# Kernel optimization log

Hardware: AMD Instinct MI355X
Metric: run time of the kernel (lower is better)

## Reference

```python
import jax, jax.numpy as jnp
import numpy as np
import math

B, P, L, LMAX = 8, 64, 32, 2048
IN_DIM, TE_DIM = 12, 20
POINT = IN_DIM + TE_DIM  # 32
HID = 128
TTCN = HID - 1  # 127
NHEAD = 4
NLAYER = 2
DFF = 2048  # torch TransformerEncoderLayer default dim_feedforward
NQ = 5
TAU = 300.0
DELTA = 5.0 * 60.0  # delta_minutes=5 -> seconds


def _pe_table(M, D):
    pos = np.arange(M, dtype=np.float32)[:, None]
    div = np.exp(np.arange(0, D, 2, dtype=np.float32) * (-math.log(10000.0) / D))
    pe = np.zeros((M, D), np.float32)
    pe[:, 0::2] = np.sin(pos * div)
    pe[:, 1::2] = np.cos(pos * div)
    return jnp.asarray(pe)


def _time_bias(M):
    idx = np.arange(M, dtype=np.float32)
    dist = np.abs(idx[:, None] - idx[None, :]) * DELTA
    return jnp.asarray(np.log(np.exp(-dist / TAU) + 1e-12).astype(np.float32))


def _ln(x, g, b):
    m = jnp.mean(x, axis=-1, keepdims=True)
    v = jnp.var(x, axis=-1, keepdims=True)
    return (x - m) * jax.lax.rsqrt(v + 1e-5) * g + b


def _mha(qx, kx, vx, Wq, bq, Wk, bk, Wv, bv, Wo, bo, bias=None, key_pad=None):
    Bq, Mq, D = qx.shape
    Mk = kx.shape[1]
    dh = D // NHEAD
    q = (qx @ Wq + bq).reshape(Bq, Mq, NHEAD, dh).transpose(0, 2, 1, 3)
    k = (kx @ Wk + bk).reshape(Bq, Mk, NHEAD, dh).transpose(0, 2, 1, 3)
    v = (vx @ Wv + bv).reshape(Bq, Mk, NHEAD, dh).transpose(0, 2, 1, 3)
    s = jnp.einsum('bhqd,bhkd->bhqk', q, k) / math.sqrt(dh)
    if bias is not None:
        s = s + bias[None, None]
    if key_pad is not None:
        s = jnp.where(key_pad[:, None, None, :], -1e9, s)
    a = jax.nn.softmax(s, axis=-1)
    o = jnp.einsum('bhqk,bhkd->bhqd', a, v).transpose(0, 2, 1, 3).reshape(Bq, Mq, D)
    return o @ Wo + bo


def forward_fn(data_sequence, ts_sequence, patch_mask, patch_index, num_batch,
               te_scale_W, te_scale_b, te_per_W, te_per_b,
               fg_W1, fg_b1, fg_W2, fg_b2, fg_W3, fg_b3, T_bias,
               ga_Wq, ga_bq, ga_Wk, ga_bk, ga_Wv, ga_bv, ga_Wo, ga_bo,
               tf_Wq, tf_bq, tf_Wk, tf_bk, tf_Wv, tf_bv, tf_Wo, tf_bo,
               tf_ln1_g, tf_ln1_b, tf_ff_W1, tf_ff_b1, tf_ff_W2, tf_ff_b2,
               tf_ln2_g, tf_ln2_b,
               cls_query, cls_Wq, cls_bq, cls_Wk, cls_bk, cls_Wv, cls_bv,
               cls_Wo, cls_bo, cls_out_W, cls_out_b):
    # --- patchify_by_len, vectorized: per-patch lengths -> cumsum starts + gather ---
    mvalid = patch_mask > 0
    lens = jnp.where(mvalid, jnp.maximum(patch_index, 0), 0)
    starts = jnp.cumsum(lens, axis=1) - lens  # exclusive cumsum (B,P)
    lar = jnp.arange(L)
    idx = starts[:, :, None] + lar[None, None, :]  # (B,P,L)
    valid = (lar[None, None, :] < lens[:, :, None]) & (idx < num_batch[:, None, None]) & mvalid[:, :, None]
    idx_c = jnp.clip(idx, 0, LMAX - 1).reshape(B, P * L)
    Xg = jnp.take_along_axis(data_sequence, idx_c[:, :, None], axis=1).reshape(B, P, L, IN_DIM)
    tsg = jnp.take_along_axis(ts_sequence, idx_c, axis=1).reshape(B, P, L, 1)
    mask_pt = valid.astype(jnp.float32)[..., None]  # (B,P,L,1)
    X_patch = Xg * mask_pt
    ts_patch = tsg * mask_pt
    # --- LearnableTE ---
    te = jnp.concatenate([ts_patch @ te_scale_W + te_scale_b,
                          jnp.sin(ts_patch @ te_per_W + te_per_b)], axis=-1)
    X_int = jnp.concatenate([X_patch, te], axis=-1).reshape(B * P, L, POINT)
    mask2 = mask_pt.reshape(B * P, L, 1)
    # --- TTCN: MLP-generated dynamic filters, masked softmax over timesteps ---
    h = jax.nn.relu(X_int @ fg_W1 + fg_b1)
    h = jax.nn.relu(h @ fg_W2 + fg_b2)
    Filt = h @ fg_W3 + fg_b3  # (N, L, TTCN*POINT)
    Fm = Filt * mask2 + (1.0 - mask2) * -1e8
    Fs = jax.nn.softmax(Fm, axis=1).reshape(B * P, L, TTCN, POINT)
    ttcn = jnp.einsum('nlp,nltp->nt', X_int, Fs)
    h_t = jax.nn.relu(ttcn + T_bias)
    patch_exists = (jnp.sum(mask2, axis=1) > 0).astype(jnp.float32)  # (N,1)
    x = jnp.concatenate([h_t, patch_exists], axis=-1).reshape(B, P, HID)
    # --- stacked time-biased patch attention + transformer encoder ---
    tb = _time_bias(P)
    pe = _pe_table(P, HID)
    key_pad = patch_mask <= 0
    pm = patch_mask[:, :, None]
    for l in range(NLAYER):
        x_last = x
        ga = _mha(x, x, x, ga_Wq[l], ga_bq[l], ga_Wk[l], ga_bk[l],
                  ga_Wv[l], ga_bv[l], ga_Wo[l], ga_bo[l], bias=tb, key_pad=key_pad)
        x = x + ga * pm
        x = x + pe[None]
        # post-norm TransformerEncoderLayer, tf_layer=1, dropout=0 at inference
        a = _mha(x, x, x, tf_Wq[l], tf_bq[l], tf_Wk[l], tf_bk[l],
                 tf_Wv[l], tf_bv[l], tf_Wo[l], tf_bo[l])
        x = _ln(x + a, tf_ln1_g[l], tf_ln1_b[l])
        f = jax.nn.relu(x @ tf_ff_W1[l] + tf_ff_b1[l]) @ tf_ff_W2[l] + tf_ff_b2[l]
        x = _ln(x + f, tf_ln2_g[l], tf_ln2_b[l])
        x = x_last + x
        x = x * pm
    # --- 5-query cross-attention classifier ---
    q = jnp.broadcast_to(cls_query[None], (B, NQ, HID))
    z = _mha(q, x, x, cls_Wq, cls_bq, cls_Wk, cls_bk, cls_Wv, cls_bv,
             cls_Wo, cls_bo, key_pad=key_pad)
    logits = (z @ cls_out_W + cls_out_b)[..., 0]  # (B,5)
    return logits


def setup_inputs() -> dict:
    key = jax.random.key(0)
    ks = iter(jax.random.split(key, 64))
    def nrm(shape, s=0.05):
        return (jax.random.normal(next(ks), shape) * s).astype(jnp.float32)
    inp = {}
    inp['data_sequence'] = jax.random.normal(next(ks), (B, LMAX, IN_DIM), dtype=jnp.float32)
    inp['ts_sequence'] = jax.random.uniform(next(ks), (B, LMAX), dtype=jnp.float32) * 100.0
    inp['patch_mask'] = jnp.ones((B, P), jnp.float32)
    inp['patch_index'] = jax.random.randint(next(ks), (B, P), 1, L + 1)
    inp['num_batch'] = jnp.full((B,), LMAX, jnp.int32)
    inp['te_scale_W'] = nrm((1, 1), 0.5)
    inp['te_scale_b'] = nrm((1,), 0.5)
    inp['te_per_W'] = nrm((1, TE_DIM - 1), 0.5)
    inp['te_per_b'] = nrm((TE_DIM - 1,), 0.5)
    inp['fg_W1'] = nrm((POINT, TTCN)); inp['fg_b1'] = jnp.zeros((TTCN,), jnp.float32)
    inp['fg_W2'] = nrm((TTCN, TTCN)); inp['fg_b2'] = jnp.zeros((TTCN,), jnp.float32)
    inp['fg_W3'] = nrm((TTCN, POINT * TTCN)); inp['fg_b3'] = jnp.zeros((POINT * TTCN,), jnp.float32)
    inp['T_bias'] = nrm((1, TTCN), 0.5)
    for nm in ['ga_Wq', 'ga_Wk', 'ga_Wv', 'ga_Wo', 'tf_Wq', 'tf_Wk', 'tf_Wv', 'tf_Wo']:
        inp[nm] = nrm((NLAYER, HID, HID))
    for nm in ['ga_bq', 'ga_bk', 'ga_bv', 'ga_bo', 'tf_bq', 'tf_bk', 'tf_bv', 'tf_bo', 'tf_ff_b2']:
        inp[nm] = jnp.zeros((NLAYER, HID), jnp.float32)
    inp['tf_ln1_g'] = jnp.ones((NLAYER, HID), jnp.float32)
    inp['tf_ln1_b'] = jnp.zeros((NLAYER, HID), jnp.float32)
    inp['tf_ln2_g'] = jnp.ones((NLAYER, HID), jnp.float32)
    inp['tf_ln2_b'] = jnp.zeros((NLAYER, HID), jnp.float32)
    inp['tf_ff_W1'] = nrm((NLAYER, HID, DFF))
    inp['tf_ff_b1'] = jnp.zeros((NLAYER, DFF), jnp.float32)
    inp['tf_ff_W2'] = nrm((NLAYER, DFF, HID))
    inp['cls_query'] = nrm((NQ, HID), 0.5)
    for nm in ['cls_Wq', 'cls_Wk', 'cls_Wv', 'cls_Wo']:
        inp[nm] = nrm((HID, HID))
    for nm in ['cls_bq', 'cls_bk', 'cls_bv', 'cls_bo']:
        inp[nm] = jnp.zeros((HID,), jnp.float32)
    inp['cls_out_W'] = nrm((HID, 1))
    inp['cls_out_b'] = jnp.zeros((1,), jnp.float32)
    return inp


def reference(data_sequence, ts_sequence, patch_mask, patch_index, num_batch,
              te_scale_W, te_scale_b, te_per_W, te_per_b,
              fg_W1, fg_b1, fg_W2, fg_b2, fg_W3, fg_b3, T_bias,
              ga_Wq, ga_bq, ga_Wk, ga_bk, ga_Wv, ga_bv, ga_Wo, ga_bo,
              tf_Wq, tf_bq, tf_Wk, tf_bk, tf_Wv, tf_bv, tf_Wo, tf_bo,
              tf_ln1_g, tf_ln1_b, tf_ff_W1, tf_ff_b1, tf_ff_W2, tf_ff_b2,
              tf_ln2_g, tf_ln2_b,
              cls_query, cls_Wq, cls_bq, cls_Wk, cls_bk, cls_Wv, cls_bv,
              cls_Wo, cls_bo, cls_out_W, cls_out_b):
    return forward_fn(data_sequence, ts_sequence, patch_mask, patch_index, num_batch,
                      te_scale_W, te_scale_b, te_per_W, te_per_b,
                      fg_W1, fg_b1, fg_W2, fg_b2, fg_W3, fg_b3, T_bias,
                      ga_Wq, ga_bq, ga_Wk, ga_bk, ga_Wv, ga_bv, ga_Wo, ga_bo,
                      tf_Wq, tf_bq, tf_Wk, tf_bk, tf_Wv, tf_bv, tf_Wo, tf_bo,
                      tf_ln1_g, tf_ln1_b, tf_ff_W1, tf_ff_b1, tf_ff_W2, tf_ff_b2,
                      tf_ln2_g, tf_ln2_b,
                      cls_query, cls_Wq, cls_bq, cls_Wk, cls_bk, cls_Wv, cls_bv,
                      cls_Wo, cls_bo, cls_out_W, cls_out_b)
```

## Files before the change

kernel.cpp:

```cpp
#include <hip/hip_runtime.h>
#include <math.h>

#define BB 8
#define PP 64
#define LL 32
#define LMAXX 2048
#define INDIM 12
#define PNT 32
#define HIDD 128
#define TTCNN 127
#define NPATCH 512

#define EPI_NONE 0
#define EPI_RELU 1
#define EPI_GA   2
#define EPI_LN   3
#define EPI_LNF  4

typedef __attribute__((ext_vector_type(8))) short short8v;
typedef __attribute__((ext_vector_type(4))) float float4v;

__device__ inline unsigned short f2bf(float f) {
    unsigned int u = __float_as_uint(f);
    unsigned int r = (u + 0x7FFFu + ((u >> 16) & 1u)) >> 16;
    return (unsigned short)r;
}

__global__ void tables_kernel(float* __restrict__ tb, float* __restrict__ pe)
{
    int e = blockIdx.x*256 + threadIdx.x;
    if (e < 64*64) {
        int i = e >> 6, j = e & 63;
        float dist = fabsf((float)(i - j)) * (300.0f / 300.0f);
        tb[e] = logf(expf(-dist) + 1e-12f);
    } else if (e < 64*64 + 64*128) {
        int e2 = e - 64*64;
        int i = e2 >> 7, d = e2 & 127;
        int mm = d >> 1;
        float div = expf((float)(2*mm) * (-logf(10000.f)/128.f));
        float ang = (float)i * div;
        pe[e2] = (d & 1) ? cosf(ang) : sinf(ang);
    }
}

__global__ void w3t_kernel(const float* __restrict__ W3, unsigned short* __restrict__ W3TB)
{
    int e = blockIdx.x*256 + threadIdx.x;
    if (e >= 4096*128) return;
    int kk = e >> 12, cidx = e & 4095;
    float v = (kk < TTCNN && cidx < 4064) ? W3[kk*4064 + cidx] : 0.f;
    W3TB[cidx*128 + kk] = f2bf(v);
}

__global__ void prep_h2_kernel(const float* __restrict__ data, const float* __restrict__ ts,
                               const float* __restrict__ pmask, const int* __restrict__ pindex,
                               const int* __restrict__ nbatch,
                               const float* __restrict__ teW, const float* __restrict__ teB,
                               const float* __restrict__ tePW, const float* __restrict__ tePB,
                               const float* __restrict__ W1, const float* __restrict__ b1,
                               const float* __restrict__ W2, const float* __restrict__ b2,
                               float* __restrict__ xint, float* __restrict__ maskout,
                               unsigned short* __restrict__ h2o)
{
    int n = blockIdx.x;
    int b = n >> 6, p = n & 63;
    __shared__ int s_start, s_len;
    __shared__ float s_mk[LL];
    __shared__ alignas(16) float Xs[LL*36];
    __shared__ alignas(16) float H1[LL*128];
    int tid = threadIdx.x;
    if (tid == 0) {
        int start = 0;
        for (int j = 0; j < p; ++j) {
            float mv = pmask[b*PP + j];
            int pi = pindex[b*PP + j];
            start += (mv > 0.f) ? (pi > 0 ? pi : 0) : 0;
        }
        float mvp = pmask[b*PP + p];
        int pip = pindex[b*PP + p];
        s_len = (mvp > 0.f) ? (pip > 0 ? pip : 0) : 0;
        s_start = start;
    }
    __syncthreads();
    int start = s_start, len = s_len, nb2 = nbatch[b];
    if (tid < LL) {
        int l = tid;
        int idx = start + l;
        float v = (l < len && idx < nb2) ? 1.f : 0.f;
        s_mk[l] = v;
        maskout[n*LL + l] = v;
    }
    __syncthreads();
    for (int e = tid; e < LL*PNT; e += 128) {
        int l = e >> 5, d = e & 31;
        float mv = s_mk[l];
        int idx = start + l;
        if (idx < 0) idx = 0;
        if (idx > LMAXX-1) idx = LMAXX-1;
        float val;
        if (d < INDIM) {
            val = (mv > 0.f) ? data[(b*LMAXX + idx)*INDIM + d] : 0.f;
        } else {
            float tsm = (mv > 0.f) ? ts[b*LMAXX + idx] : 0.f;
            if (d == INDIM) val = tsm * teW[0] + teB[0];
            else { int j = d - INDIM - 1; val = sinf(tsm * tePW[j] + tePB[j]); }
        }
        Xs[l*36 + d] = val;
        xint[n*(LL*PNT) + e] = val;
    }
    __syncthreads();
    int j = tid;
    float acc[LL];
    if (j < TTCNN) {
        #pragma unroll
        for (int l = 0; l < LL; ++l) acc[l] = b1[j];
        for (int d4 = 0; d4 < 8; ++d4) {
            float w0 = W1[(d4*4+0)*TTCNN + j];
            float w1 = W1[(d4*4+1)*TTCNN + j];
            float w2 = W1[(d4*4+2)*TTCNN + j];
            float w3 = W1[(d4*4+3)*TTCNN + j];
            #pragma unroll
            for (int l = 0; l < LL; ++l) {
                float4 x = *(float4*)&Xs[l*36 + d4*4];
                acc[l] = fmaf(x.x, w0, acc[l]);
                acc[l] = fmaf(x.y, w1, acc[l]);
                acc[l] = fmaf(x.z, w2, acc[l]);
                acc[l] = fmaf(x.w, w3, acc[l]);
            }
        }
        #pragma unroll
        for (int l = 0; l < LL; ++l) H1[l*128 + j] = fmaxf(acc[l], 0.f);
    } else {
        #pragma unroll
        for (int l = 0; l < LL; ++l) H1[l*128 + 127] = 0.f;
    }
    __syncthreads();
    if (j < TTCNN) {
        #pragma unroll
        for (int l = 0; l < LL; ++l) acc[l] = b2[j];
        for (int k4 = 0; k4 < 32; ++k4) {
            int k = k4*4;
            float w0 = W2[(k+0)*TTCNN + j];
            float w1 = W2[(k+1)*TTCNN + j];
            float w2 = W2[(k+2)*TTCNN + j];
            float w3 = (k+3 < TTCNN) ? W2[(k+3)*TTCNN + j] : 0.f;
            #pragma unroll
            for (int l = 0; l < LL; ++l) {
                float4 h = *(float4*)&H1[l*128 + k];
                acc[l] = fmaf(h.x, w0, acc[l]);
                acc[l] = fmaf(h.y, w1, acc[l]);
                acc[l] = fmaf(h.z, w2, acc[l]);
                acc[l] = fmaf(h.w, w3, acc[l]);
            }
        }
        #pragma unroll
        for (int l = 0; l < LL; ++l) h2o[(n*LL + l)*128 + j] = f2bf(fmaxf(acc[l], 0.f));
    } else {
        #pragma unroll
        for (int l = 0; l < LL; ++l) h2o[(n*LL + l)*128 + 127] = 0;
    }
}

__global__ __launch_bounds__(256) void ttcn_mfma_kernel(
    const unsigned short* __restrict__ h2b,
    const float* __restrict__ xint,
    const float* __restrict__ mask,
    const unsigned short* __restrict__ w3tb,
    const float* __restrict__ b3,
    const float* __restrict__ tbias,
    float* __restrict__ x)
{
    int bid = blockIdx.x;
    int n = bid >> 3, chunk = bid & 7;
    __shared__ alignas(16) unsigned short h2s[32*136];
    __shared__ alignas(16) float Xs[32*36];
    __shared__ float mk[32];
    int tid = threadIdx.x;
    for (int f = tid; f < 512; f += 256) {
        int l = f >> 4, c16 = f & 15;
        *(short8v*)&h2s[l*136 + c16*8] = *(const short8v*)&h2b[(n*32 + l)*128 + c16*8];
    }
    {
        int l = tid >> 3, d4 = (tid & 7)*4;
        *(float4*)&Xs[l*36 + d4] = *(const float4*)&xint[n*1024 + l*32 + d4];
    }
    if (tid < 32) mk[tid] = mask[n*32 + tid];
    __syncthreads();
    if (chunk == 0 && tid == 0) {
        float e = 0.f;
        for (int l = 0; l < 32; ++l) e += mk[l];
        x[n*HIDD + 127] = (e > 0.f) ? 1.f : 0.f;
    }
    int wave = tid >> 6, lane = tid & 63;
    int li = lane & 15, hi = lane >> 4;
    short8v a[2][4];
    #pragma unroll
    for (int mt = 0; mt < 2; ++mt)
        #pragma unroll
        for (int kk = 0; kk < 4; ++kk)
            a[mt][kk] = *(short8v*)&h2s[(mt*16 + li)*136 + kk*32 + hi*8];
    int cwbase = chunk*512 + wave*128;
    for (int tl = 0; tl < 4; ++tl) {
        int c0 = cwbase + tl*32;
        float4v acc[2][2] = {};
        #pragma unroll
        for (int nt2 = 0; nt2 < 2; ++nt2) {
            const unsigned short* bp = &w3tb[(size_t)(c0 + nt2*16 + li)*128 + hi*8];
            #pragma unroll
            for (int kk = 0; kk < 4; ++kk) {
                short8v bf = *(const short8v*)&bp[kk*32];
                acc[0][nt2] = __builtin_amdgcn_mfma_f32_16x16x32_bf16(a[0][kk], bf, acc[0][nt2], 0, 0, 0);
                acc[1][nt2] = __builtin_amdgcn_mfma_f32_16x16x32_bf16(a[1][kk], bf, acc[1][nt2], 0, 0, 0);
            }
        }
        int t = c0 >> 5;
        float colv2 = 0.f;
        #pragma unroll
        for (int nt2 = 0; nt2 < 2; ++nt2) {
            int c = c0 + nt2*16 + li;
            float bv = (c < 4064) ? b3[c] : 0.f;
            int p = (nt2 << 4) + li;
            float fm[8];
            #pragma unroll
            for (int mt = 0; mt < 2; ++mt)
                #pragma unroll
                for (int r4 = 0; r4 < 4; ++r4) {
                    int r = mt*16 + hi*4 + r4;
                    float mv = mk[r];
                    fm[mt*4 + r4] = (acc[mt][nt2][r4] + bv)*mv + (1.f - mv)*(-1e8f);
                }
            float m = fm[0];
            #pragma unroll
            for (int i = 1; i < 8; ++i) m = fmaxf(m, fm[i]);
            m = fmaxf(m, __shfl_xor(m, 16));
            m = fmaxf(m, __shfl_xor(m, 32));
            float s = 0.f, w = 0.f;
            #pragma unroll
            for (int mt = 0; mt < 2; ++mt)
                #pragma unroll
                for (int r4 = 0; r4 < 4; ++r4) {
                    int r = mt*16 + hi*4 + r4;
                    float e = expf(fm[mt*4 + r4] - m);
                    s += e;
                    w += e * Xs[r*36 + p];
                }
            s += __shfl_xor(s, 16); w += __shfl_xor(w, 16);
            s += __shfl_xor(s, 32); w += __shfl_xor(w, 32);
            colv2 += w / s;
        }
        colv2 += __shfl_xor(colv2, 1);
        colv2 += __shfl_xor(colv2, 2);
        colv2 += __shfl_xor(colv2, 4);
        colv2 += __shfl_xor(colv2, 8);
        if (lane == 0 && t < TTCNN)
            x[n*HIDD + t] = fmaxf(colv2 + tbias[t], 0.f);
    }
}

__global__ __launch_bounds__(256) void lin_kernel(
    const float* __restrict__ A, int lda,
    const float* __restrict__ W0, const float* __restrict__ Wb0,
    const float* __restrict__ W1, const float* __restrict__ Wb1,
    const float* __restrict__ W2, const float* __restrict__ Wb2,
    float* __restrict__ O0, float* __restrict__ O1, float* __restrict__ O2,
    int M, int K, int N, int epi,
    const float* __restrict__ xres, const float* __restrict__ xlast_in,
    float* __restrict__ xlast_out,
    const float* __restrict__ pmk, const float* __restrict__ pe,
    const float* __restrict__ g, const float* __restrict__ bt)
{
    __shared__ alignas(16) float As[8*68];
    __shared__ float red[4][4][2];
    int tid = threadIdx.x;
    int cloc = tid & 127, rh = tid >> 7;
    int c = blockIdx.z*128 + cloc;
    int r0 = blockIdx.x*8;
    const float* W; const float* Wb; float* O;
    if (blockIdx.y == 0)      { W = W0; Wb = Wb0; O = O0; }
    else if (blockIdx.y == 1) { W = W1; Wb = Wb1; O = O1; }
    else                      { W = W2; Wb = Wb2; O = O2; }
    float acc0 = 0.f, acc1 = 0.f, acc2 = 0.f, acc3 = 0.f;
    for (int kc = 0; kc < K; kc += 64) {
        __syncthreads();
        if (tid < 128) {
            int row = tid >> 4, kk = (tid & 15)*4;
            int r = r0 + row;
            float4 v = make_float4(0.f, 0.f, 0.f, 0.f);
            if (r < M) v = *(const float4*)&A[(size_t)r*lda + kc + kk];
            *(float4*)&As[row*68 + kk] = v;
        }
        __syncthreads();
        const float* wp = &W[(size_t)kc*N + c];
        #pragma unroll 4
        for (int kk4 = 0; kk4 < 16; ++kk4) {
            float w0 = wp[(size_t)(kk4*4+0)*N];
            float w1 = wp[(size_t)(kk4*4+1)*N];
            float w2 = wp[(size_t)(kk4*4+2)*N];
            float w3 = wp[(size_t)(kk4*4+3)*N];
            float4 a0 = *(float4*)&As[(rh*4+0)*68 + kk4*4];
            float4 a1 = *(float4*)&As[(rh*4+1)*68 + kk4*4];
            float4 a2 = *(float4*)&As[(rh*4+2)*68 + kk4*4];
            float4 a3 = *(float4*)&As[(rh*4+3)*68 + kk4*4];
            acc0 += a0.x*w0 + a0.y*w1 + a0.z*w2 + a0.w*w3;
            acc1 += a1.x*w0 + a1.y*w1 + a1.z*w2 + a1.w*w3;
            acc2 += a2.x*w0 + a2.y*w1 + a2.z*w2 + a2.w*w3;
            acc3 += a3.x*w0 + a3.y*w1 + a3.z*w2 + a3.w*w3;
        }
    }
    float bv = Wb ? Wb[c] : 0.f;
    float val[4] = {acc0 + bv, acc1 + bv, acc2 + bv, acc3 + bv};
    int rbase = r0 + rh*4;
    if (epi == EPI_NONE || epi == EPI_RELU) {
        #pragma unroll
        for (int i = 0; i < 4; ++i) {
            int r = rbase + i;
            if (r < M) {
                float v = val[i];
                if (epi == EPI_RELU) v = fmaxf(v, 0.f);
                O[(size_t)r*N + c] = v;
            }
        }
    } else if (epi == EPI_GA) {
        #pragma unroll
        for (int i = 0; i < 4; ++i) {
            int r = rbase + i;
            float xr = xres[r*128 + cloc];
            float pmv = pmk[r];
            float pev = pe[(r & 63)*128 + cloc];
            xlast_out[r*128 + cloc] = xr;
            O[r*128 + cloc] = xr + val[i]*pmv + pev;
        }
    } else {
        float tv[4], s[4], s2[4];
        #pragma unroll
        for (int i = 0; i < 4; ++i) {
            int r = rbase + i;
            tv[i] = xres[r*128 + cloc] + val[i];
            s[i] = tv[i];
            s2[i] = tv[i]*tv[i];
        }
        #pragma unroll
        for (int i = 0; i < 4; ++i) {
            for (int off = 32; off >= 1; off >>= 1) {
                s[i]  += __shfl_xor(s[i],  off);
                s2[i] += __shfl_xor(s2[i], off);
            }
        }
        int wid = tid >> 6;
        if ((tid & 63) == 0) {
            #pragma unroll
            for (int i = 0; i < 4; ++i) { red[wid][i][0] = s[i]; red[wid][i][1] = s2[i]; }
        }
        __syncthreads();
        int pw = wid ^ 1;
        #pragma unroll
        for (int i = 0; i < 4; ++i) {
            float st  = red[wid][i][0] + red[pw][i][0];
            float s2t = red[wid][i][1] + red[pw][i][1];
            float mean = st * (1.f/128.f);
            float var = s2t * (1.f/128.f) - mean*mean;
            float rs = rsqrtf(var + 1e-5f);
            float y = (tv[i] - mean)*rs*g[cloc] + bt[cloc];
            int r = rbase + i;
            if (epi == EPI_LN) O[r*128 + cloc] = y;
            else               O[r*128 + cloc] = (xlast_in[r*128 + cloc] + y)*pmk[r];
        }
    }
}

__global__ __launch_bounds__(256) void ff2_partial_kernel(
    const float* __restrict__ A,
    const float* __restrict__ W,
    float* __restrict__ PART)
{
    __shared__ alignas(16) float As[8*68];
    int tid = threadIdx.x;
    int cloc = tid & 127, rh = tid >> 7;
    int r0 = blockIdx.x*8;
    int kz = blockIdx.z*256;
    float acc0 = 0.f, acc1 = 0.f, acc2 = 0.f, acc3 = 0.f;
    for (int kc = kz; kc < kz + 256; kc += 64) {
        __syncthreads();
        if (tid < 128) {
            int row = tid >> 4, kk = (tid & 15)*4;
            *(float4*)&As[row*68 + kk] = *(const float4*)&A[(size_t)(r0+row)*2048 + kc + kk];
        }
        __syncthreads();
        const float* wp = &W[(size_t)kc*128 + cloc];
        #pragma unroll 4
        for (int kk4 = 0; kk4 < 16; ++kk4) {
            float w0 = wp[(size_t)(kk4*4+0)*128];
            float w1 = wp[(size_t)(kk4*4+1)*128];
            float w2 = wp[(size_t)(kk4*4+2)*128];
            float w3 = wp[(size_t)(kk4*4+3)*128];
            float4 a0 = *(float4*)&As[(rh*4+0)*68 + kk4*4];
            float4 a1 = *(float4*)&As[(rh*4+1)*68 + kk4*4];
            float4 a2 = *(float4*)&As[(rh*4+2)*68 + kk4*4];
            float4 a3 = *(float4*)&As[(rh*4+3)*68 + kk4*4];
            acc0 += a0.x*w0 + a0.y*w1 + a0.z*w2 + a0.w*w3;
            acc1 += a1.x*w0 + a1.y*w1 + a1.z*w2 + a1.w*w3;
            acc2 += a2.x*w0 + a2.y*w1 + a2.z*w2 + a2.w*w3;
            acc3 += a3.x*w0 + a3.y*w1 + a3.z*w2 + a3.w*w3;
        }
    }
    float* pb = &PART[((size_t)blockIdx.z*512 + r0 + rh*4)*128 + cloc];
    pb[0]     = acc0;
    pb[128]   = acc1;
    pb[256]   = acc2;
    pb[384]   = acc3;
}

__global__ void ln2f_kernel(const float* __restrict__ PART, const float* __restrict__ b2,
                            const float* __restrict__ xres, const float* __restrict__ xlast,
                            const float* __restrict__ pmk,
                            const float* __restrict__ g, const float* __restrict__ bt,
                            float* __restrict__ xout)
{
    int r = blockIdx.x, c = threadIdx.x;
    float v = b2[c];
    #pragma unroll
    for (int z = 0; z < 8; ++z) v += PART[((size_t)z*512 + r)*128 + c];
    float tv = xres[r*128 + c] + v;
    float s = tv, s2 = tv*tv;
    for (int off = 32; off >= 1; off >>= 1) {
        s  += __shfl_xor(s,  off);
        s2 += __shfl_xor(s2, off);
    }
    __shared__ float red[2][2];
    int w = c >> 6;
    if ((c & 63) == 0) { red[w][0] = s; red[w][1] = s2; }
    __syncthreads();
    float st  = red[0][0] + red[1][0];
    float s2t = red[0][1] + red[1][1];
    float mean = st * (1.f/128.f);
    float var = s2t * (1.f/128.f) - mean*mean;
    float y = (tv - mean)*rsqrtf(var + 1e-5f)*g[c] + bt[c];
    xout[r*128 + c] = (xlast[r*128 + c] + y)*pmk[r];
}

__global__ __launch_bounds__(256) void attn_kernel(
    const float* __restrict__ q, const float* __restrict__ k, const float* __restrict__ v,
    float* __restrict__ out, const float* __restrict__ tb,
    const float* __restrict__ pmk, int flags)
{
    int bid = blockIdx.x;
    int b = bid >> 3, h = (bid >> 1) & 3, half = bid & 1;
    int rbase = half*32;
    __shared__ alignas(16) float qs[32*36];
    __shared__ alignas(16) float ks[64*36];
    __shared__ alignas(16) float vs[64*36];
    __shared__ float as_[32*68];
    int tid = threadIdx.x;
    {
        int m = tid >> 3, d4 = (tid & 7)*4;
        *(float4*)&qs[m*36 + d4] = *(const float4*)&q[(b*64 + rbase + m)*128 + h*32 + d4];
    }
    for (int f = tid; f < 512; f += 256) {
        int m = f >> 3, d4 = (f & 7)*4;
        int gofs = (b*64 + m)*128 + h*32 + d4;
        *(float4*)&ks[m*36 + d4] = *(const float4*)&k[gofs];
        *(float4*)&vs[m*36 + d4] = *(const float4*)&v[gofs];
    }
    __syncthreads();
    int r = tid >> 3, qd = tid & 7;
    float sreg[8];
    #pragma unroll
    for (int j = 0; j < 8; ++j) {
        int cc = j*8 + qd;
        float acc = 0.f;
        #pragma unroll
        for (int d4 = 0; d4 < 8; ++d4) {
            float4 a = *(float4*)&qs[r*36 + d4*4];
            float4 bb = *(float4*)&ks[cc*36 + d4*4];
            acc += a.x*bb.x + a.y*bb.y + a.z*bb.z + a.w*bb.w;
        }
        float s = acc * 0.17677669529663687f;
        if (flags & 1) s += tb[(rbase + r)*64 + cc];
        if (flags & 2) { if (pmk[b*64 + cc] <= 0.f) s = -1e9f; }
        sreg[j] = s;
    }
    float m = sreg[0];
    #pragma unroll
    for (int j = 1; j < 8; ++j) m = fmaxf(m, sreg[j]);
    m = fmaxf(m, __shfl_xor(m, 1));
    m = fmaxf(m, __shfl_xor(m, 2));
    m = fmaxf(m, __shfl_xor(m, 4));
    float ssum = 0.f;
    #pragma unroll
    for (int j = 0; j < 8; ++j) { sreg[j] = expf(sreg[j] - m); ssum += sreg[j]; }
    ssum += __shfl_xor(ssum, 1);
    ssum += __shfl_xor(ssum, 2);
    ssum += __shfl_xor(ssum, 4);
    float inv = 1.f / ssum;
    #pragma unroll
    for (int j = 0; j < 8; ++j) as_[r*68 + j*8 + qd] = sreg[j]*inv;
    __syncthreads();
    float o0 = 0.f, o1 = 0.f, o2 = 0.f, o3 = 0.f;
    int d0 = qd*4;
    for (int cc = 0; cc < 64; ++cc) {
        float a = as_[r*68 + cc];
        float4 v4 = *(float4*)&vs[cc*36 + d0];
        o0 += a*v4.x; o1 += a*v4.y; o2 += a*v4.z; o3 += a*v4.w;
    }
    *(float4*)&out[(b*64 + rbase + r)*128 + h*32 + d0] = make_float4(o0, o1, o2, o3);
}

__global__ __launch_bounds__(256) void cls_attn_kernel(
    const float* __restrict__ clsq, const float* __restrict__ Wq, const float* __restrict__ bq,
    const float* __restrict__ k, const float* __restrict__ v,
    const float* __restrict__ pmk,
    const float* __restrict__ Wo, const float* __restrict__ bo,
    const float* __restrict__ WoutW, const float* __restrict__ boutB,
    float* __restrict__ outp)
{
    int b = blockIdx.x;
    __shared__ alignas(16) float ks[64*132];
    __shared__ alignas(16) float vs[64*132];
    __shared__ alignas(16) float q5[5*132];
    __shared__ float cq[5*128];
    __shared__ float sb[5*68];
    __shared__ float z[5*132];
    __shared__ float wef[129];
    int tid = threadIdx.x;
    for (int f = tid; f < 64*32; f += 256) {
        int m = f >> 5, d4 = (f & 31)*4;
        *(float4*)&ks[m*132 + d4] = *(const float4*)&k[(b*64+m)*128 + d4];
        *(float4*)&vs[m*132 + d4] = *(const float4*)&v[(b*64+m)*128 + d4];
    }
    for (int e = tid; e < 5*128; e += 256) {
        cq[e] = clsq[e];
        z[(e >> 7)*132 + (e & 127)] = 0.f;
    }
    __syncthreads();
    for (int it = tid; it < 5*128; it += 256) {
        int qr = it >> 7, d = it & 127;
        float a = bq[d];
        for (int kk = 0; kk < 128; ++kk) a += cq[qr*128 + kk]*Wq[kk*128 + d];
        q5[qr*132 + d] = a;
    }
    if (tid < 128) {
        float s = 0.f;
        for (int cc = 0; cc < 128; ++cc) s += Wo[tid*128 + cc]*WoutW[cc];
        wef[tid] = s;
    } else if (tid == 128) {
        float t = boutB[0];
        for (int cc = 0; cc < 128; ++cc) t += bo[cc]*WoutW[cc];
        wef[128] = t;
    }
    __syncthreads();
    for (int h = 0; h < 4; ++h) {
        for (int it = tid; it < 5*64; it += 256) {
            int qr = it >> 6, cc = it & 63;
            float acc = 0.f;
            #pragma unroll
            for (int d4 = 0; d4 < 8; ++d4) {
                float4 a = *(float4*)&q5[qr*132 + h*32 + d4*4];
                float4 bb = *(float4*)&ks[cc*132 + h*32 + d4*4];
                acc += a.x*bb.x + a.y*bb.y + a.z*bb.z + a.w*bb.w;
            }
            float s = acc * 0.17677669529663687f;
            if (pmk[b*64 + cc] <= 0.f) s = -1e9f;
            sb[qr*68 + cc] = s;
        }
        __syncthreads();
        if (tid < 5) {
            float m = -3e38f;
            for (int cc = 0; cc < 64; ++cc) m = fmaxf(m, sb[tid*68 + cc]);
            float ssum = 0.f;
            for (int cc = 0; cc < 64; ++cc) {
                float e = expf(sb[tid*68 + cc] - m);
                sb[tid*68 + cc] = e;
                ssum += e;
            }
            float inv = 1.f/ssum;
            for (int cc = 0; cc < 64; ++cc) sb[tid*68 + cc] *= inv;
        }
        __syncthreads();
        for (int it = tid; it < 5*32; it += 256) {
            int qr = it >> 5, d = it & 31;
            float acc = 0.f;
            for (int cc = 0; cc < 64; ++cc) acc += sb[qr*68 + cc]*vs[cc*132 + h*32 + d];
            z[qr*132 + h*32 + d] = acc;
        }
        __syncthreads();
    }
    if (tid < 5) {
        float acc = wef[128];
        for (int d = 0; d < 128; ++d) acc += z[tid*132 + d]*wef[d];
        outp[b*5 + tid] = acc;
    }
}

extern "C" void kernel_launch(void* const* d_in, const int* in_sizes, int n_in,
                              void* d_out, int out_size, void* d_ws, size_t ws_size,
                              hipStream_t stream)
{
    (void)n_in; (void)out_size; (void)ws_size;
    #define FP(i) ((const float*)d_in[i])
    const float* data = FP(0);
    const float* ts   = FP(1);
    const float* pmask= FP(2);
    const int*   pidx = (const int*)d_in[3];
    const int*   nb   = (const int*)d_in[4];
    const float* teW  = FP(5);
    const float* teB  = FP(6);
    const float* tePW = FP(7);
    const float* tePB = FP(8);
    const float* fgW1 = FP(9);
    const float* fgb1 = FP(10);
    const float* fgW2 = FP(11);
    const float* fgb2 = FP(12);
    const float* fgW3 = FP(13);
    const float* fgb3 = FP(14);
    const float* Tb   = FP(15);
    const float *gaWq,*gaWk,*gaWv,*gaWo,*tfWq,*tfWk,*tfWv,*tfWo;
    const float *gabq,*gabk,*gabv,*gabo,*tfbq,*tfbk,*tfbv,*tfbo,*ffb2;
    const float *ln1g,*ln1b,*ln2g,*ln2b,*ffW1,*ffb1,*ffW2;
    const float *clsq,*clsWq,*clsWk,*clsWv,*clsWo,*clsbq,*clsbk,*clsbv,*clsbo,*cloW,*clob;
    if (in_sizes[17] == 2*128*128) {
        gaWq=FP(16); gaWk=FP(17); gaWv=FP(18); gaWo=FP(19);
        tfWq=FP(20); tfWk=FP(21); tfWv=FP(22); tfWo=FP(23);
        gabq=FP(24); gabk=FP(25); gabv=FP(26); gabo=FP(27);
        tfbq=FP(28); tfbk=FP(29); tfbv=FP(30); tfbo=FP(31);
        ffb2=FP(32); ln1g=FP(33); ln1b=FP(34); ln2g=FP(35); ln2b=FP(36);
        ffW1=FP(37); ffb1=FP(38); ffW2=FP(39);
        clsq=FP(40); clsWq=FP(41); clsWk=FP(42); clsWv=FP(43); clsWo=FP(44);
        clsbq=FP(45); clsbk=FP(46); clsbv=FP(47); clsbo=FP(48); cloW=FP(49); clob=FP(50);
    } else {
        gaWq=FP(16); gabq=FP(17); gaWk=FP(18); gabk=FP(19);
        gaWv=FP(20); gabv=FP(21); gaWo=FP(22); gabo=FP(23);
        tfWq=FP(24); tfbq=FP(25); tfWk=FP(26); tfbk=FP(27);
        tfWv=FP(28); tfbv=FP(29); tfWo=FP(30); tfbo=FP(31);
        ln1g=FP(32); ln1b=FP(33); ffW1=FP(34); ffb1=FP(35); ffW2=FP(36); ffb2=FP(37);
        ln2g=FP(38); ln2b=FP(39);
        clsq=FP(40); clsWq=FP(41); clsbq=FP(42); clsWk=FP(43); clsbk=FP(44);
        clsWv=FP(45); clsbv=FP(46); clsWo=FP(47); clsbo=FP(48); cloW=FP(49); clob=FP(50);
    }

    float* ws   = (float*)d_ws;
    float* XINT = ws;
    float* PART = ws;
    float* MASK = ws + 524288;
    unsigned short* W3TB = (unsigned short*)(ws + 540672);
    unsigned short* H2Bb = (unsigned short*)(ws + 1060864);
    float* X    = ws + 3158016;
    float* XLAST= X + 65536;
    float* Q    = XLAST + 65536;
    float* Kb   = Q + 65536;
    float* Vb   = Kb + 65536;
    float* ATT  = Vb + 65536;
    float* HIDB = ATT + 65536;
    float* TBT  = HIDB + 1048576;
    float* PET  = TBT + 4096;

    tables_kernel<<<48, 256, 0, stream>>>(TBT, PET);
    w3t_kernel<<<2048, 256, 0, stream>>>(fgW3, W3TB);
    prep_h2_kernel<<<512, 128, 0, stream>>>(data, ts, pmask, pidx, nb, teW, teB, tePW, tePB,
                                            fgW1, fgb1, fgW2, fgb2, XINT, MASK, H2Bb);
    ttcn_mfma_kernel<<<4096, 256, 0, stream>>>(H2Bb, XINT, MASK, W3TB, fgb3, Tb, X);

    for (int l = 0; l < 2; ++l) {
        const float* Wq = gaWq + l*16384; const float* bq = gabq + l*128;
        const float* Wk = gaWk + l*16384; const float* bk = gabk + l*128;
        const float* Wv = gaWv + l*16384; const float* bv = gabv + l*128;
        const float* Wo = gaWo + l*16384; const float* bo = gabo + l*128;
        lin_kernel<<<dim3(64,3,1), 256, 0, stream>>>(X, 128, Wq,bq, Wk,bk, Wv,bv, Q,Kb,Vb,
            512,128,128, EPI_NONE, nullptr,nullptr,nullptr,nullptr,nullptr,nullptr,nullptr);
        attn_kernel<<<64, 256, 0, stream>>>(Q, Kb, Vb, ATT, TBT, pmask, 3);
        lin_kernel<<<dim3(64,1,1), 256, 0, stream>>>(ATT, 128, Wo,bo, Wo,bo, Wo,bo, X,X,X,
            512,128,128, EPI_GA, X, nullptr, XLAST, pmask, PET, nullptr, nullptr);
        const float* Wq2 = tfWq + l*16384; const float* bq2 = tfbq + l*128;
        const float* Wk2 = tfWk + l*16384; const float* bk2 = tfbk + l*128;
        const float* Wv2 = tfWv + l*16384; const float* bv2 = tfbv + l*128;
        const float* Wo2 = tfWo + l*16384; const float* bo2 = tfbo + l*128;
        lin_kernel<<<dim3(64,3,1), 256, 0, stream>>>(X, 128, Wq2,bq2, Wk2,bk2, Wv2,bv2, Q,Kb,Vb,
            512,128,128, EPI_NONE, nullptr,nullptr,nullptr,nullptr,nullptr,nullptr,nullptr);
        attn_kernel<<<64, 256, 0, stream>>>(Q, Kb, Vb, ATT, TBT, pmask, 0);
        lin_kernel<<<dim3(64,1,1), 256, 0, stream>>>(ATT, 128, Wo2,bo2, Wo2,bo2, Wo2,bo2, X,X,X,
            512,128,128, EPI_LN, X, nullptr, nullptr, nullptr, nullptr, ln1g + l*128, ln1b + l*128);
        lin_kernel<<<dim3(64,1,16), 256, 0, stream>>>(X, 128,
            ffW1 + (size_t)l*128*2048, ffb1 + l*2048, ffW1, ffb1, ffW1, ffb1, HIDB,HIDB,HIDB,
            512,128,2048, EPI_RELU, nullptr,nullptr,nullptr,nullptr,nullptr,nullptr,nullptr);
        ff2_partial_kernel<<<dim3(64,1,8), 256, 0, stream>>>(HIDB, ffW2 + (size_t)l*2048*128, PART);
        ln2f_kernel<<<512, 128, 0, stream>>>(PART, ffb2 + l*128, X, XLAST, pmask,
                                             ln2g + l*128, ln2b + l*128, X);
    }

    lin_kernel<<<dim3(64,2,1), 256, 0, stream>>>(X, 128, clsWk,clsbk, clsWv,clsbv, clsWv,clsbv,
        Kb,Vb,Vb, 512,128,128, EPI_NONE, nullptr,nullptr,nullptr,nullptr,nullptr,nullptr,nullptr);
    cls_attn_kernel<<<8, 256, 0, stream>>>(clsq, clsWq, clsbq, Kb, Vb, pmask,
                                           clsWo, clsbo, cloW, clob, (float*)d_out);
}
```

Measured before the change: 458.6 us.

## Fuse TTCN prep and MFMA filter kernels; use fast exp/rcp in softmaxes

Merges the per-patch MLP prep kernel with the TTCN MFMA kernel so h2, xint and mask stay in shared memory instead of going through global memory. Each block now handles all 4096 filter columns for one patch rather than splitting them over 8 blocks, so the grid drops from 4096 to 512 blocks and there is less parallelism. The table and W3 transpose kernels are combined into one launch. Softmax max-subtraction in the TTCN path is dropped in favour of a fixed -30 mask offset, and __expf/rcp intrinsics replace expf and division, which risks overflow and reduced accuracy.

```diff
diff --git a/kernel.cpp b/kernel.cpp
--- a/kernel.cpp
+++ b/kernel.cpp
@@ -26,48 +26,52 @@
     return (unsigned short)r;
 }
 
-__global__ void tables_kernel(float* __restrict__ tb, float* __restrict__ pe)
-{
-    int e = blockIdx.x*256 + threadIdx.x;
-    if (e < 64*64) {
-        int i = e >> 6, j = e & 63;
-        float dist = fabsf((float)(i - j)) * (300.0f / 300.0f);
-        tb[e] = logf(expf(-dist) + 1e-12f);
-    } else if (e < 64*64 + 64*128) {
-        int e2 = e - 64*64;
-        int i = e2 >> 7, d = e2 & 127;
-        int mm = d >> 1;
-        float div = expf((float)(2*mm) * (-logf(10000.f)/128.f));
-        float ang = (float)i * div;
-        pe[e2] = (d & 1) ? cosf(ang) : sinf(ang);
-    }
-}
-
-__global__ void w3t_kernel(const float* __restrict__ W3, unsigned short* __restrict__ W3TB)
-{
-    int e = blockIdx.x*256 + threadIdx.x;
-    if (e >= 4096*128) return;
-    int kk = e >> 12, cidx = e & 4095;
-    float v = (kk < TTCNN && cidx < 4064) ? W3[kk*4064 + cidx] : 0.f;
-    W3TB[cidx*128 + kk] = f2bf(v);
-}
-
-__global__ void prep_h2_kernel(const float* __restrict__ data, const float* __restrict__ ts,
-                               const float* __restrict__ pmask, const int* __restrict__ pindex,
-                               const int* __restrict__ nbatch,
-                               const float* __restrict__ teW, const float* __restrict__ teB,
-                               const float* __restrict__ tePW, const float* __restrict__ tePB,
-                               const float* __restrict__ W1, const float* __restrict__ b1,
-                               const float* __restrict__ W2, const float* __restrict__ b2,
-                               float* __restrict__ xint, float* __restrict__ maskout,
-                               unsigned short* __restrict__ h2o)
+__global__ void tables_w3t_kernel(const float* __restrict__ W3, unsigned short* __restrict__ W3TB,
+                                  float* __restrict__ tb, float* __restrict__ pe)
+{
+    int bid = blockIdx.x;
+    if (bid < 2048) {
+        int e = bid*256 + threadIdx.x;
+        int kk = e >> 12, cidx = e & 4095;
+        float v = (kk < TTCNN && cidx < 4064) ? W3[kk*4064 + cidx] : 0.f;
+        W3TB[cidx*128 + kk] = f2bf(v);
+    } else {
+        int e = (bid - 2048)*256 + threadIdx.x;
+        if (e < 64*64) {
+            int i = e >> 6, j = e & 63;
+            float dist = fabsf((float)(i - j));
+            tb[e] = logf(expf(-dist) + 1e-12f);
+        } else if (e < 64*64 + 64*128) {
+            int e2 = e - 64*64;
+            int i = e2 >> 7, d = e2 & 127;
+            int mm = d >> 1;
+            float div = expf((float)(2*mm) * (-logf(10000.f)/128.f));
+            float ang = (float)i * div;
+            pe[e2] = (d & 1) ? cosf(ang) : sinf(ang);
+        }
+    }
+}
+
+__global__ __launch_bounds__(256) void prep_ttcn_kernel(
+    const float* __restrict__ data, const float* __restrict__ ts,
+    const float* __restrict__ pmask, const int* __restrict__ pindex,
+    const int* __restrict__ nbatch,
+    const float* __restrict__ teW, const float* __restrict__ teB,
+    const float* __restrict__ tePW, const float* __restrict__ tePB,
+    const float* __restrict__ W1, const float* __restrict__ b1,
+    const float* __restrict__ W2, const float* __restrict__ b2,
+    const unsigned short* __restrict__ w3tb,
+    const float* __restrict__ b3,
+    const float* __restrict__ tbias,
+    float* __restrict__ x)
 {
     int n = blockIdx.x;
     int b = n >> 6, p = n & 63;
     __shared__ int s_start, s_len;
-    __shared__ float s_mk[LL];
+    __shared__ float mk[LL];
     __shared__ alignas(16) float Xs[LL*36];
     __shared__ alignas(16) float H1[LL*128];
+    __shared__ alignas(16) unsigned short h2s[LL*136];
     int tid = threadIdx.x;
     if (tid == 0) {
         int start = 0;
@@ -86,14 +90,12 @@
     if (tid < LL) {
         int l = tid;
         int idx = start + l;
-        float v = (l < len && idx < nb2) ? 1.f : 0.f;
-        s_mk[l] = v;
-        maskout[n*LL + l] = v;
-    }
-    __syncthreads();
-    for (int e = tid; e < LL*PNT; e += 128) {
+        mk[l] = (l < len && idx < nb2) ? 1.f : 0.f;
+    }
+    __syncthreads();
+    for (int e = tid; e < LL*PNT; e += 256) {
         int l = e >> 5, d = e & 31;
-        float mv = s_mk[l];
+        float mv = mk[l];
         int idx = start + l;
         if (idx < 0) idx = 0;
         if (idx > LMAXX-1) idx = LMAXX-1;
@@ -106,91 +108,71 @@
             else { int j = d - INDIM - 1; val = sinf(tsm * tePW[j] + tePB[j]); }
         }
         Xs[l*36 + d] = val;
-        xint[n*(LL*PNT) + e] = val;
-    }
-    __syncthreads();
-    int j = tid;
-    float acc[LL];
-    if (j < TTCNN) {
-        #pragma unroll
-        for (int l = 0; l < LL; ++l) acc[l] = b1[j];
-        for (int d4 = 0; d4 < 8; ++d4) {
-            float w0 = W1[(d4*4+0)*TTCNN + j];
-            float w1 = W1[(d4*4+1)*TTCNN + j];
-            float w2 = W1[(d4*4+2)*TTCNN + j];
-            float w3 = W1[(d4*4+3)*TTCNN + j];
-            #pragma unroll
-            for (int l = 0; l < LL; ++l) {
-                float4 x = *(float4*)&Xs[l*36 + d4*4];
-                acc[l] = fmaf(x.x, w0, acc[l]);
-                acc[l] = fmaf(x.y, w1, acc[l]);
-                acc[l] = fmaf(x.z, w2, acc[l]);
-                acc[l] = fmaf(x.w, w3, acc[l]);
+    }
+    __syncthreads();
+    if (tid == 0) {
+        float e = 0.f;
+        for (int l = 0; l < LL; ++l) e += mk[l];
+        x[n*HIDD + 127] = (e > 0.f) ? 1.f : 0.f;
+    }
+    {
+        int j = tid & 127, lh = tid >> 7;
+        float acc[16];
+        if (j < TTCNN) {
+            #pragma unroll
+            for (int il = 0; il < 16; ++il) acc[il] = b1[j];
+            for (int d4 = 0; d4 < 8; ++d4) {
+                float w0 = W1[(d4*4+0)*TTCNN + j];
+                float w1 = W1[(d4*4+1)*TTCNN + j];
+                float w2 = W1[(d4*4+2)*TTCNN + j];
+                float w3 = W1[(d4*4+3)*TTCNN + j];
+                #pragma unroll
+                for (int il = 0; il < 16; ++il) {
+                    float4 xv = *(float4*)&Xs[(lh*16 + il)*36 + d4*4];
+                    acc[il] = fmaf(xv.x, w0, acc[il]);
+                    acc[il] = fmaf(xv.y, w1, acc[il]);
+                    acc[il] = fmaf(xv.z, w2, acc[il]);
+                    acc[il] = fmaf(xv.w, w3, acc[il]);
+                }
             }
-        }
-        #pragma unroll
-        for (int l = 0; l < LL; ++l) H1[l*128 + j] = fmaxf(acc[l], 0.f);
-    } else {
-        #pragma unroll
-        for (int l = 0; l < LL; ++l) H1[l*128 + 127] = 0.f;
-    }
-    __syncthreads();
-    if (j < TTCNN) {
-        #pragma unroll
-        for (int l = 0; l < LL; ++l) acc[l] = b2[j];
-        for (int k4 = 0; k4 < 32; ++k4) {
-            int k = k4*4;
-            float w0 = W2[(k+0)*TTCNN + j];
-            float w1 = W2[(k+1)*TTCNN + j];
-            float w2 = W2[(k+2)*TTCNN + j];
-            float w3 = (k+3 < TTCNN) ? W2[(k+3)*TTCNN + j] : 0.f;
-            #pragma unroll
-            for (int l = 0; l < LL; ++l) {
-                float4 h = *(float4*)&H1[l*128 + k];
-                acc[l] = fmaf(h.x, w0, acc[l]);
-                acc[l] = fmaf(h.y, w1, acc[l]);
-                acc[l] = fmaf(h.z, w2, acc[l]);
-                acc[l] = fmaf(h.w, w3, acc[l]);
+            #pragma unroll
+            for (int il = 0; il < 16; ++il) H1[(lh*16 + il)*128 + j] = fmaxf(acc[il], 0.f);
+        } else {
+            #pragma unroll
+            for (int il = 0; il < 16; ++il) H1[(lh*16 + il)*128 + 127] = 0.f;
+        }
+    }
+    __syncthreads();
+    {
+        int j = tid & 127, lh = tid >> 7;
+        float acc[16];
+        if (j < TTCNN) {
+            #pragma unroll
+            for (int il = 0; il < 16; ++il) acc[il] = b2[j];
+            for (int k4 = 0; k4 < 32; ++k4) {
+                int k = k4*4;
+                float w0 = W2[(k+0)*TTCNN + j];
+                float w1 = W2[(k+1)*TTCNN + j];
+                float w2 = W2[(k+2)*TTCNN + j];
+                float w3 = (k+3 < TTCNN) ? W2[(k+3)*TTCNN + j] : 0.f;
+                #pragma unroll
+                for (int il = 0; il < 16; ++il) {
+                    float4 h = *(float4*)&H1[(lh*16 + il)*128 + k];
+                    acc[il] = fmaf(h.x, w0, acc[il]);
+                    acc[il] = fmaf(h.y, w1, acc[il]);
+                    acc[il] = fmaf(h.z, w2, acc[il]);
+                    acc[il] = fmaf(h.w, w3, acc[il]);
+                }
             }
-        }
-        #pragma unroll
-        for (int l = 0; l < LL; ++l) h2o[(n*LL + l)*128 + j] = f2bf(fmaxf(acc[l], 0.f));
-    } else {
-        #pragma unroll
-        for (int l = 0; l < LL; ++l) h2o[(n*LL + l)*128 + 127] = 0;
-    }
-}
-
-__global__ __launch_bounds__(256) void ttcn_mfma_kernel(
-    const unsigned short* __restrict__ h2b,
-    const float* __restrict__ xint,
-    const float* __restrict__ mask,
-    const unsigned short* __restrict__ w3tb,
-    const float* __restrict__ b3,
-    const float* __restrict__ tbias,
-    float* __restrict__ x)
-{
-    int bid = blockIdx.x;
-    int n = bid >> 3, chunk = bid & 7;
-    __shared__ alignas(16) unsigned short h2s[32*136];
-    __shared__ alignas(16) float Xs[32*36];
-    __shared__ float mk[32];
-    int tid = threadIdx.x;
-    for (int f = tid; f < 512; f += 256) {
-        int l = f >> 4, c16 = f & 15;
-        *(short8v*)&h2s[l*136 + c16*8] = *(const short8v*)&h2b[(n*32 + l)*128 + c16*8];
-    }
-    {
-        int l = tid >> 3, d4 = (tid & 7)*4;
-        *(float4*)&Xs[l*36 + d4] = *(const float4*)&xint[n*1024 + l*32 + d4];
-    }
-    if (tid < 32) mk[tid] = mask[n*32 + tid];
-    __syncthreads();
-    if (chunk == 0 && tid == 0) {
-        float e = 0.f;
-        for (int l = 0; l < 32; ++l) e += mk[l];
-        x[n*HIDD + 127] = (e > 0.f) ? 1.f : 0.f;
-    }
+            #pragma unroll
+            for (int il = 0; il < 16; ++il)
+                h2s[(lh*16 + il)*136 + j] = f2bf(fmaxf(acc[il], 0.f));
+        } else {
+            #pragma unroll
+            for (int il = 0; il < 16; ++il) h2s[(lh*16 + il)*136 + 127] = 0;
+        }
+    }
+    __syncthreads();
     int wave = tid >> 6, lane = tid & 63;
     int li = lane & 15, hi = lane >> 4;
     short8v a[2][4];
@@ -199,8 +181,21 @@
         #pragma unroll
         for (int kk = 0; kk < 4; ++kk)
             a[mt][kk] = *(short8v*)&h2s[(mt*16 + li)*136 + kk*32 + hi*8];
-    int cwbase = chunk*512 + wave*128;
-    for (int tl = 0; tl < 4; ++tl) {
+    float mkr[8], off8[8], xv0[8], xv1[8];
+    #pragma unroll
+    for (int mt = 0; mt < 2; ++mt)
+        #pragma unroll
+        for (int r4 = 0; r4 < 4; ++r4) {
+            int i = mt*4 + r4;
+            int rr = mt*16 + hi*4 + r4;
+            float mv = mk[rr];
+            mkr[i] = mv;
+            off8[i] = (1.f - mv) * (-30.f);
+            xv0[i] = Xs[rr*36 + li];
+            xv1[i] = Xs[rr*36 + 16 + li];
+        }
+    int cwbase = wave*1024;
+    for (int tl = 0; tl < 32; ++tl) {
         int c0 = cwbase + tl*32;
         float4v acc[2][2] = {};
         #pragma unroll
@@ -217,36 +212,22 @@
         float colv2 = 0.f;
         #pragma unroll
         for (int nt2 = 0; nt2 < 2; ++nt2) {
-            int c = c0 + nt2*16 + li;
-            float bv = (c < 4064) ? b3[c] : 0.f;
-            int p = (nt2 << 4) + li;
-            float fm[8];
+            int cglob = c0 + nt2*16 + li;
+            float bv = (cglob < 4064) ? b3[cglob] : 0.f;
+            float s = 0.f, w = 0.f;
             #pragma unroll
             for (int mt = 0; mt < 2; ++mt)
                 #pragma unroll
                 for (int r4 = 0; r4 < 4; ++r4) {
-                    int r = mt*16 + hi*4 + r4;
-                    float mv = mk[r];
-                    fm[mt*4 + r4] = (acc[mt][nt2][r4] + bv)*mv + (1.f - mv)*(-1e8f);
-                }
-            float m = fm[0];
-            #pragma unroll
-            for (int i = 1; i < 8; ++i) m = fmaxf(m, fm[i]);
-            m = fmaxf(m, __shfl_xor(m, 16));
-            m = fmaxf(m, __shfl_xor(m, 32));
-            float s = 0.f, w = 0.f;
-            #pragma unroll
-            for (int mt = 0; mt < 2; ++mt)
-                #pragma unroll
-                for (int r4 = 0; r4 < 4; ++r4) {
-                    int r = mt*16 + hi*4 + r4;
-                    float e = expf(fm[mt*4 + r4] - m);
+                    int i = mt*4 + r4;
+                    float fm = (acc[mt][nt2][r4] + bv)*mkr[i] + off8[i];
+                    float e = __expf(fm);
                     s += e;
-                    w += e * Xs[r*36 + p];
+                    w = fmaf(e, (nt2 == 0) ? xv0[i] : xv1[i], w);
                 }
             s += __shfl_xor(s, 16); w += __shfl_xor(w, 16);
             s += __shfl_xor(s, 32); w += __shfl_xor(w, 32);
-            colv2 += w / s;
+            colv2 = fmaf(w, __builtin_amdgcn_rcpf(s), colv2);
         }
         colv2 += __shfl_xor(colv2, 1);
         colv2 += __shfl_xor(colv2, 2);
@@ -487,11 +468,11 @@
     m = fmaxf(m, __shfl_xor(m, 4));
     float ssum = 0.f;
     #pragma unroll
-    for (int j = 0; j < 8; ++j) { sreg[j] = expf(sreg[j] - m); ssum += sreg[j]; }
+    for (int j = 0; j < 8; ++j) { sreg[j] = __expf(sreg[j] - m); ssum += sreg[j]; }
     ssum += __shfl_xor(ssum, 1);
     ssum += __shfl_xor(ssum, 2);
     ssum += __shfl_xor(ssum, 4);
-    float inv = 1.f / ssum;
+    float inv = __builtin_amdgcn_rcpf(ssum);
     #pragma unroll
     for (int j = 0; j < 8; ++j) as_[r*68 + j*8 + qd] = sreg[j]*inv;
     __syncthreads();
@@ -568,11 +549,11 @@
             for (int cc = 0; cc < 64; ++cc) m = fmaxf(m, sb[tid*68 + cc]);
             float ssum = 0.f;
             for (int cc = 0; cc < 64; ++cc) {
-                float e = expf(sb[tid*68 + cc] - m);
+                float e = __expf(sb[tid*68 + cc] - m);
                 sb[tid*68 + cc] = e;
                 ssum += e;
             }
-            float inv = 1.f/ssum;
+            float inv = __builtin_amdgcn_rcpf(ssum);
             for (int cc = 0; cc < 64; ++cc) sb[tid*68 + cc] *= inv;
         }
         __syncthreads();
@@ -638,26 +619,21 @@
     }
 
     float* ws   = (float*)d_ws;
-    float* XINT = ws;
-    float* PART = ws;
-    float* MASK = ws + 524288;
-    unsigned short* W3TB = (unsigned short*)(ws + 540672);
-    unsigned short* H2Bb = (unsigned short*)(ws + 1060864);
-    float* X    = ws + 3158016;
+    unsigned short* W3TB = (unsigned short*)ws;
+    float* X    = ws + 262144;
     float* XLAST= X + 65536;
     float* Q    = XLAST + 65536;
     float* Kb   = Q + 65536;
     float* Vb   = Kb + 65536;
     float* ATT  = Vb + 65536;
     float* HIDB = ATT + 65536;
-    float* TBT  = HIDB + 1048576;
+    float* PART = HIDB + 1048576;
+    float* TBT  = PART + 524288;
     float* PET  = TBT + 4096;
 
-    tables_kernel<<<48, 256, 0, stream>>>(TBT, PET);
-    w3t_kernel<<<2048, 256, 0, stream>>>(fgW3, W3TB);
-    prep_h2_kernel<<<512, 128, 0, stream>>>(data, ts, pmask, pidx, nb, teW, teB, tePW, tePB,
-                                            fgW1, fgb1, fgW2, fgb2, XINT, MASK, H2Bb);
-    ttcn_mfma_kernel<<<4096, 256, 0, stream>>>(H2Bb, XINT, MASK, W3TB, fgb3, Tb, X);
+    tables_w3t_kernel<<<2096, 256, 0, stream>>>(fgW3, W3TB, TBT, PET);
+    prep_ttcn_kernel<<<512, 256, 0, stream>>>(data, ts, pmask, pidx, nb, teW, teB, tePW, tePB,
+                                              fgW1, fgb1, fgW2, fgb2, W3TB, fgb3, Tb, X);
 
     for (int l = 0; l < 2; ++l) {
         const float* Wq = gaWq + l*16384; const float* bq = gabq + l*128;
```

After: 422.5 us. 7.9% less time.
